# Kernel tuning notes

Measured on AMD Instinct MI355X. Metric: run time of the kernel, lower is better.

## Reference

```python
import jax, jax.numpy as jnp
import numpy as np

K = 4194304  # number of AR-GAS prediction steps


def _update_student(y, mu, sigma2, a_mu, a_s, b_mu, b_s, w_mu, w_s, nu, strength):
    """One GAS Student-t score-driven update (scalar math)."""
    a_mu = a_mu * strength
    a_s = a_s * strength
    r = y - mu
    inv_nu = 1.0 / nu
    denom = 1.0 + r * r * inv_nu / sigma2  # 1 + (y-mu)^2 / (nu*sigma2)
    scale = (1.0 + inv_nu) / denom
    mu_upd = mu + a_mu * scale * r
    s2_upd = sigma2 + a_s * (scale * r * r - sigma2)
    mu_new = w_mu + b_mu * mu_upd
    s2_new = w_s + b_s * s2_upd
    return mu_new, s2_new


def setup_inputs() -> dict:
    key = jax.random.key(0)
    return {
        "deep_preds": jax.random.normal(key, (K,), dtype=jnp.float32),
        "last_mu": jnp.float32(0.1),
        "last_sigma": jnp.float32(1.0),   # treated as variance (sqrt taken at the end)
        "alpha_mu": jnp.float32(0.05),
        "alpha_sigma": jnp.float32(0.05),
        "beta_mu": jnp.float32(0.98),
        "beta_sigma": jnp.float32(0.98),
        "omega_mu": jnp.float32(0.0),
        "omega_sigma": jnp.float32(0.02),
        "nu": jnp.float32(5.0),
        "norm_strength": jnp.float32(1.0),
    }


def reference(deep_preds, last_mu, last_sigma, alpha_mu, alpha_sigma,
              beta_mu, beta_sigma, omega_mu, omega_sigma, nu, norm_strength):
    # use_deep_preds=True path: step i consumes deep_preds[i] and the previous state
    def step(carry, y):
        mu, s2 = carry
        mu2, s22 = _update_student(y, mu, s2, alpha_mu, alpha_sigma,
                                   beta_mu, beta_sigma, omega_mu, omega_sigma,
                                   nu, norm_strength)
        return (mu2, s22), (mu2, s22)

    _, (mu_pred, s2_pred) = jax.lax.scan(step, (last_mu, last_sigma), deep_preds)
    return mu_pred, jnp.sqrt(s2_pred)
```

## Files before the change

kernel.cpp:

```cpp
#include <hip/hip_runtime.h>
#include <math.h>


#define CHUNK  32
#define BURN   96
#define NRUN   (BURN / 32)
#define BLOCK  256
#define OUTW   (BLOCK * CHUNK)
#define REGION (OUTW + BURN)
#define SWZ(e) ((e) + 4 * ((e) >> 5))
#define SY_PAD 9320
#define SZ_PAD 9216

__global__ __launch_bounds__(BLOCK, 2)
void ar_gas_kernel(const float* __restrict__ y,
                   const float* __restrict__ p_last_mu,
                   const float* __restrict__ p_last_s2,
                   const float* __restrict__ p_amu,
                   const float* __restrict__ p_as,
                   const float* __restrict__ p_bmu,
                   const float* __restrict__ p_bs,
                   const float* __restrict__ p_wmu,
                   const float* __restrict__ p_ws,
                   const float* __restrict__ p_nu,
                   const float* __restrict__ p_str,
                   float* __restrict__ out,
                   int n)
{
    __shared__ __align__(16) float sy[SY_PAD];
    __shared__ __align__(16) float sz[SZ_PAD];
    const int t     = threadIdx.x;
    const int blk   = blockIdx.x;
    const int gbase = blk * OUTW - BURN;

    const float nu       = *p_nu;
    const float strength = *p_str;
    const float a_mu = (*p_amu) * strength;
    const float a_s  = (*p_as)  * strength;
    const float b_mu = *p_bmu;
    const float b_s  = *p_bs;
    const float w_mu = *p_wmu;
    const float w_s  = *p_ws;

    const float inv_nu = __builtin_amdgcn_rcpf(nu);
    const float k1   = (nu + 1.0f) * inv_nu;
    const float bamk = b_mu * a_mu * k1;
    const float bask = nu * b_s * a_s * k1;
    const float c3   = b_s * (1.0f - a_s);
    const float wsn  = nu * w_s;

    #pragma unroll
    for (int it = 0; it < 9; ++it) {
        int idx = (t + BLOCK * it) * 4;
        if (idx < REGION) {
            int g = gbase + idx;
            float4 v = make_float4(0.f, 0.f, 0.f, 0.f);
            if (g >= 0) v = *(const float4*)(y + g);
            *(float4*)(sy + SWZ(idx)) = v;
        }
    }
    __syncthreads();

    int skipR = 0;
    float mu, u;
    if (blk == 0 && t <= NRUN) {
        mu    = *p_last_mu;
        u     = nu * (*p_last_s2);
        skipR = NRUN - t;
    } else {
        mu = w_mu * __builtin_amdgcn_rcpf(fmaxf(1.0f - b_mu, 1e-12f));
        u  = wsn  * __builtin_amdgcn_rcpf(fmaxf(1.0f - b_s,  1e-12f));
    }
    const float muS = mu, uS = u;

#define STEP(yv) do {                                   \
        float r   = (yv) - mu;                          \
        float den = fmaf(r, r, u);                      \
        float inv = __builtin_amdgcn_rcpf(den);         \
        float t2  = (u * r) * inv;                      \
        mu = fmaf(bamk, t2, fmaf(b_mu, mu, w_mu));      \
        u  = fmaf(bask, t2 * r, fmaf(c3, u, wsn));      \
    } while (0)
#define LDRUN(B, off) do { _Pragma("unroll")                         \
        for (int k = 0; k < 8; ++k)                                  \
            B[k] = *(const float4*)(sy + (off) + 4 * k); } while (0)
#define RUN32(B) do { _Pragma("unroll")                              \
        for (int k = 0; k < 8; ++k) {                                \
            STEP(B[k].x); STEP(B[k].y); STEP(B[k].z); STEP(B[k].w);  \
        } } while (0)

    const int b0 = 36 * t;
    float4 P[8], Q[8];
    LDRUN(P, b0);
    LDRUN(Q, b0 + 36);
    RUN32(P);  if (0 < skipR) { mu = muS; u = uS; }
    LDRUN(P, b0 + 72);
    RUN32(Q);  if (1 < skipR) { mu = muS; u = uS; }
    LDRUN(Q, b0 + 108);
    RUN32(P);  if (2 < skipR) { mu = muS; u = uS; }

    __syncthreads();

    {
        const int pe = b0 + 108;
        const int ze = b0;
        float4 m, s;
        #pragma unroll
        for (int q = 0; q < 8; ++q) {
            STEP(Q[q].x); m.x = mu; s.x = __builtin_amdgcn_sqrtf(u * inv_nu);
            STEP(Q[q].y); m.y = mu; s.y = __builtin_amdgcn_sqrtf(u * inv_nu);
            STEP(Q[q].z); m.z = mu; s.z = __builtin_amdgcn_sqrtf(u * inv_nu);
            STEP(Q[q].w); m.w = mu; s.w = __builtin_amdgcn_sqrtf(u * inv_nu);
            *(float4*)(sy + pe + 4 * q) = m;
            *(float4*)(sz + ze + 4 * q) = s;
        }
    }
#undef RUN32
#undef LDRUN
#undef STEP
    __syncthreads();

    const int obase = blk * OUTW;
    #pragma unroll
    for (int it = 0; it < 8; ++it) {
        int idx = (t + BLOCK * it) * 4;
        int f   = SWZ(idx) + 108;
        int fz  = SWZ(idx);
        *(float4*)(out + obase + idx) =
            make_float4(sy[f], sy[f + 1], sy[f + 2], sy[f + 3]);
        *(float4*)(out + n + obase + idx) =
            make_float4(sz[fz], sz[fz + 1], sz[fz + 2], sz[fz + 3]);
    }
}

extern "C" void kernel_launch(void* const* d_in, const int* in_sizes, int n_in,
                              void* d_out, int out_size, void* d_ws, size_t ws_size,
                              hipStream_t stream) {
    const float* y = (const float*)d_in[0];
    const int n    = in_sizes[0];
    const int grid = n / OUTW;

    ar_gas_kernel<<<grid, BLOCK, 0, stream>>>(
        y,
        (const float*)d_in[1],
        (const float*)d_in[2],
        (const float*)d_in[3],
        (const float*)d_in[4],
        (const float*)d_in[5],
        (const float*)d_in[6],
        (const float*)d_in[7],
        (const float*)d_in[8],
        (const float*)d_in[9],
        (const float*)d_in[10],
        (float*)d_out, n);
}
```

Baseline: 97.42 us.

## Halve per-thread chunk to 16 steps with burn-in over six runs

Each thread now produces 16 outputs instead of 32 while keeping a 96-step burn-in, so the grid doubles and occupancy hint rises to 4 blocks per CU. Shared memory shrinks and swizzles are adjusted per stride. This trades more redundant burn-in work per output (96 warmup steps for 16 outputs) for more parallel threads to hide the serial recurrence latency.

```diff
diff --git a/kernel.cpp b/kernel.cpp
--- a/kernel.cpp
+++ b/kernel.cpp
@@ -2,17 +2,18 @@
 #include <math.h>
 
 
-#define CHUNK  32
+#define CHUNK  16
 #define BURN   96
-#define NRUN   (BURN / 32)
+#define NRUN   (BURN / CHUNK)
 #define BLOCK  256
 #define OUTW   (BLOCK * CHUNK)
 #define REGION (OUTW + BURN)
-#define SWZ(e) ((e) + 4 * ((e) >> 5))
-#define SY_PAD 9320
-#define SZ_PAD 9216
+#define SWZ(e)  ((e) + 4 * ((e) >> 4))
+#define SWZ32(e) ((e) + 4 * ((e) >> 5))
+#define SY_PAD 5240
+#define SZ_PAD 4608
 
-__global__ __launch_bounds__(BLOCK, 2)
+__global__ __launch_bounds__(BLOCK, 4)
 void ar_gas_kernel(const float* __restrict__ y,
                    const float* __restrict__ p_last_mu,
                    const float* __restrict__ p_last_s2,
@@ -50,7 +51,7 @@
     const float wsn  = nu * w_s;
 
     #pragma unroll
-    for (int it = 0; it < 9; ++it) {
+    for (int it = 0; it < 5; ++it) {
         int idx = (t + BLOCK * it) * 4;
         if (idx < REGION) {
             int g = gbase + idx;
@@ -82,53 +83,59 @@
         u  = fmaf(bask, t2 * r, fmaf(c3, u, wsn));      \
     } while (0)
 #define LDRUN(B, off) do { _Pragma("unroll")                         \
-        for (int k = 0; k < 8; ++k)                                  \
+        for (int k = 0; k < 4; ++k)                                  \
             B[k] = *(const float4*)(sy + (off) + 4 * k); } while (0)
-#define RUN32(B) do { _Pragma("unroll")                              \
-        for (int k = 0; k < 8; ++k) {                                \
+#define RUN16(B) do { _Pragma("unroll")                              \
+        for (int k = 0; k < 4; ++k) {                                \
             STEP(B[k].x); STEP(B[k].y); STEP(B[k].z); STEP(B[k].w);  \
         } } while (0)
 
-    const int b0 = 36 * t;
-    float4 P[8], Q[8];
-    LDRUN(P, b0);
-    LDRUN(Q, b0 + 36);
-    RUN32(P);  if (0 < skipR) { mu = muS; u = uS; }
-    LDRUN(P, b0 + 72);
-    RUN32(Q);  if (1 < skipR) { mu = muS; u = uS; }
-    LDRUN(Q, b0 + 108);
-    RUN32(P);  if (2 < skipR) { mu = muS; u = uS; }
+    const int q0 = 20 * t;
+    float4 P[4], Q[4];
+    LDRUN(P, q0);
+    LDRUN(Q, q0 + 20);
+    RUN16(P);  if (0 < skipR) { mu = muS; u = uS; }
+    LDRUN(P, q0 + 40);
+    RUN16(Q);  if (1 < skipR) { mu = muS; u = uS; }
+    LDRUN(Q, q0 + 60);
+    RUN16(P);  if (2 < skipR) { mu = muS; u = uS; }
+    LDRUN(P, q0 + 80);
+    RUN16(Q);  if (3 < skipR) { mu = muS; u = uS; }
+    LDRUN(Q, q0 + 100);
+    RUN16(P);  if (4 < skipR) { mu = muS; u = uS; }
+    LDRUN(P, q0 + 120);
+    RUN16(Q);  if (5 < skipR) { mu = muS; u = uS; }
 
     __syncthreads();
 
     {
-        const int pe = b0 + 108;
-        const int ze = b0;
+        const int pe = q0 + 120;
+        const int ze = 16 * t + 4 * (t >> 1);
         float4 m, s;
         #pragma unroll
-        for (int q = 0; q < 8; ++q) {
-            STEP(Q[q].x); m.x = mu; s.x = __builtin_amdgcn_sqrtf(u * inv_nu);
-            STEP(Q[q].y); m.y = mu; s.y = __builtin_amdgcn_sqrtf(u * inv_nu);
-            STEP(Q[q].z); m.z = mu; s.z = __builtin_amdgcn_sqrtf(u * inv_nu);
-            STEP(Q[q].w); m.w = mu; s.w = __builtin_amdgcn_sqrtf(u * inv_nu);
-            *(float4*)(sy + pe + 4 * q) = m;
-            *(float4*)(sz + ze + 4 * q) = s;
+        for (int g = 0; g < 4; ++g) {
+            STEP(P[g].x); m.x = mu; s.x = __builtin_amdgcn_sqrtf(u * inv_nu);
+            STEP(P[g].y); m.y = mu; s.y = __builtin_amdgcn_sqrtf(u * inv_nu);
+            STEP(P[g].z); m.z = mu; s.z = __builtin_amdgcn_sqrtf(u * inv_nu);
+            STEP(P[g].w); m.w = mu; s.w = __builtin_amdgcn_sqrtf(u * inv_nu);
+            *(float4*)(sy + pe + 4 * g) = m;
+            *(float4*)(sz + ze + 4 * g) = s;
         }
     }
-#undef RUN32
+#undef RUN16
 #undef LDRUN
 #undef STEP
     __syncthreads();
 
     const int obase = blk * OUTW;
     #pragma unroll
-    for (int it = 0; it < 8; ++it) {
-        int idx = (t + BLOCK * it) * 4;
-        int f   = SWZ(idx) + 108;
-        int fz  = SWZ(idx);
-        *(float4*)(out + obase + idx) =
+    for (int it = 0; it < 4; ++it) {
+        int o  = (t + BLOCK * it) * 4;
+        int f  = SWZ(o) + 120;
+        int fz = SWZ32(o);
+        *(float4*)(out + obase + o) =
             make_float4(sy[f], sy[f + 1], sy[f + 2], sy[f + 3]);
-        *(float4*)(out + n + obase + idx) =
+        *(float4*)(out + n + obase + o) =
             make_float4(sz[fz], sz[fz + 1], sz[fz + 2], sz[fz + 3]);
     }
 }
```

Result: slower. 99.96 us (+2.6%).
